# Performance work log

Hardware: AMD Instinct MI355X
Metric: run time of the kernel (lower is better)

Reference implementation:

```python
import jax, jax.numpy as jnp
import numpy as np

N_NODES = 100000
N_EDGES = 1600000
IN_C, HID_C, OUT_C = 128, 128, 40


def setup_inputs() -> dict:
    key = jax.random.key(0)
    ks = jax.random.split(key, 8)
    sd_in = 1.0 / np.sqrt(IN_C)
    sd_hid = 1.0 / np.sqrt(HID_C)
    return {
        "x": jax.random.normal(ks[0], (N_NODES, IN_C), dtype=jnp.float32),
        "edge_index": jax.random.randint(ks[1], (2, N_EDGES), 0, N_NODES, dtype=jnp.int64),
        # layer 1: lin_l (aggregated neighbors, with bias), lin_r (root, no bias)
        "W1l": jax.random.uniform(ks[2], (IN_C, HID_C), jnp.float32, -sd_in, sd_in),
        "W1r": jax.random.uniform(ks[3], (IN_C, HID_C), jnp.float32, -sd_in, sd_in),
        "b1": jnp.zeros((HID_C,), jnp.float32),
        # layer 2
        "W2l": jax.random.uniform(ks[4], (HID_C, OUT_C), jnp.float32, -sd_hid, sd_hid),
        "W2r": jax.random.uniform(ks[5], (HID_C, OUT_C), jnp.float32, -sd_hid, sd_hid),
        "b2": jnp.zeros((OUT_C,), jnp.float32),
    }


def _sage_conv(x, src, dst, Wl, Wr, b, num_nodes):
    # mean aggregation of source-node messages at destination nodes
    msg = x[src]                                          # [E, d] gather
    agg = jax.ops.segment_sum(msg, dst, num_segments=num_nodes)  # [N, d]
    cnt = jax.ops.segment_sum(jnp.ones((src.shape[0],), x.dtype), dst,
                              num_segments=num_nodes)     # [N]
    agg = agg / jnp.maximum(cnt, 1.0)[:, None]
    # lin_l(agg) + lin_r(x)  (bias lives in lin_l, matching PyG SAGEConv)
    return agg @ Wl + x @ Wr + b


def reference(x, edge_index, W1l, W1r, b1, W2l, W2r, b2):
    n = x.shape[0]
    src, dst = edge_index[0], edge_index[1]  # messages flow src -> dst
    h = jax.nn.relu(_sage_conv(x, src, dst, W1l, W1r, b1, n))
    # dropout p=0.0 -> identity
    out = _sage_conv(h, src, dst, W2l, W2r, b2, n)
    return jax.nn.log_softmax(out, axis=-1)
```

## Files before the change

### kernel.cpp

```cpp
#include <hip/hip_runtime.h>
#include <stdint.h>


typedef unsigned int uint32;
typedef unsigned short u16;
typedef __bf16 bf16x8 __attribute__((ext_vector_type(8)));
typedef float  f32x4  __attribute__((ext_vector_type(4)));
typedef unsigned short u16x8 __attribute__((ext_vector_type(8)));

#define CAPB 96
#define MAXE 2592
#define MAXN 104
#define RSST 112

__device__ __forceinline__ float bf2f(u16 u) {
    union { uint32 i; float f; } v; v.i = ((uint32)u) << 16; return v.f;
}
__device__ __forceinline__ u16 f2bf(float f) {
    union { float f; uint32 i; } v; v.f = f;
    uint32 i = v.i;
    uint32 r = (i + 0x7FFFu + ((i >> 16) & 1u)) >> 16;
    return (u16)r;
}

__global__ void k_prep(const float* __restrict__ W1l, const float* __restrict__ W1r,
                       const float* __restrict__ W2l, const float* __restrict__ W2r,
                       u16* __restrict__ Wt1, u16* __restrict__ Wt2,
                       int* __restrict__ gcur1, int cap1,
                       int* __restrict__ gcur2, int cap2) {
    if (blockIdx.x == 0 && threadIdx.x < 8) gcur1[threadIdx.x] = threadIdx.x * cap1;
    if (blockIdx.x < 4) {
        int idx = blockIdx.x * 256 + threadIdx.x;
        gcur2[idx] = idx * cap2;
    }
    if (blockIdx.x < 128) {
        int idx = blockIdx.x * 256 + threadIdx.x;
        int c = idx >> 7, k = idx & 127;
        float v = (c < 128) ? W1l[k * 128 + c] : W1r[k * 128 + (c - 128)];
        Wt1[idx] = f2bf(v);
    } else {
        int idx = (blockIdx.x - 128) * 256 + threadIdx.x;
        int c = idx >> 7, k = idx & 127;
        const float* W = (c < 48) ? W2l : W2r;
        int cc = (c < 48) ? c : c - 48;
        float v = (cc < 40) ? W[k * 40 + cc] : 0.f;
        Wt2[idx] = f2bf(v);
    }
}

__global__ __launch_bounds__(512) void k_fused1(
        const int* __restrict__ src, const int* __restrict__ dst,
        uint32* __restrict__ part, int* __restrict__ gcur,
        int E, int sw, uint32 magic, int cap, int nt1,
        const float* __restrict__ x, const u16* __restrict__ Wt,
        u16* __restrict__ z1, u16* __restrict__ r1, int N) {
    int tid = threadIdx.x;
    if ((int)blockIdx.x < nt1) {
        __shared__ uint32 buf[2048];
        __shared__ int cnt8[8][8];
        __shared__ int base8[8][8];
        __shared__ int bstart[8], bn[8], gbase[8];
        int rep = tid & 7;
        int tile = blockIdx.x;
        if (tid < 64) cnt8[tid >> 3][tid & 7] = 0;
        __syncthreads();
        int e0 = (tile << 11) + tid * 4;
        int bk[4]; uint32 pk[4]; int nv = 0;
        if (e0 + 3 < E) {
            int4 d4 = *(const int4*)(dst + e0);
            int4 s4 = *(const int4*)(src + e0);
            int dd[4] = {d4.x, d4.y, d4.z, d4.w};
            int ss[4] = {s4.x, s4.y, s4.z, s4.w};
            nv = 4;
#pragma unroll
            for (int k = 0; k < 4; ++k) {
                bk[k] = (int)(((unsigned long long)(uint32)dd[k] * magic) >> 32);
                pk[k] = ((uint32)ss[k] << 14) | (uint32)(dd[k] - bk[k] * sw);
            }
        } else {
            for (int e = e0; e < E && e < e0 + 4; ++e) {
                int d = dst[e];
                int b = (int)(((unsigned long long)(uint32)d * magic) >> 32);
                bk[nv] = b;
                pk[nv] = ((uint32)src[e] << 14) | (uint32)(d - b * sw);
                ++nv;
            }
        }
        for (int k = 0; k < nv; ++k) atomicAdd(&cnt8[bk[k]][rep], 1);
        __syncthreads();
        if (tid == 0) {
            int run = 0;
            for (int b = 0; b < 8; ++b) {
                bstart[b] = run; int t0 = run;
                for (int r = 0; r < 8; ++r) { base8[b][r] = run; run += cnt8[b][r]; }
                bn[b] = run - t0;
            }
        }
        __syncthreads();
        if (tid < 64) cnt8[tid >> 3][tid & 7] = base8[tid >> 3][tid & 7];
        __syncthreads();
        for (int k = 0; k < nv; ++k) {
            int pos = atomicAdd(&cnt8[bk[k]][rep], 1);
            buf[pos] = pk[k];
        }
        if (tid < 8 && bn[tid] > 0)
            gbase[tid] = atomicAdd(&gcur[tid], bn[tid]);
        __syncthreads();
#pragma unroll
        for (int b = 0; b < 8; ++b) {
            int n = bn[b];
            if (n == 0) continue;
            int gb = gbase[b], bs = bstart[b];
            int lim = (b + 1) * cap;
            for (int i = tid; i < n; i += 512) {
                int p = gb + i;
                if (p < lim) part[p] = buf[bs + i];
            }
        }
    } else {
        __shared__ u16 xs[128][136];
        int rbase = ((int)blockIdx.x - nt1) * 128;
#pragma unroll
        for (int i = 0; i < 8; ++i) {
            int fi = tid + i * 512;
            int row = fi >> 5, c4 = fi & 31;
            int grow = rbase + row;
            grow = grow < N ? grow : N - 1;
            float4 v = *(const float4*)(x + ((size_t)grow << 7) + c4 * 4);
            ushort4 w4;
            w4.x = f2bf(v.x); w4.y = f2bf(v.y); w4.z = f2bf(v.z); w4.w = f2bf(v.w);
            *(ushort4*)&xs[row][c4 * 4] = w4;
        }

        int lane = tid & 63;
        int w    = tid >> 6;
        int l15 = lane & 15, g = lane >> 4;
        int rloc = (w >> 2) * 64;
        int cbase = (w & 3) * 64;

        bf16x8 Bf[4][4];
#pragma unroll
        for (int c = 0; c < 4; ++c)
#pragma unroll
            for (int ks = 0; ks < 4; ++ks)
                Bf[c][ks] = *(const bf16x8*)(Wt + (((size_t)(cbase + c * 16 + l15)) << 7)
                                                + ks * 32 + g * 8);

        f32x4 acc[4][4];
        f32x4 z4 = {0.f, 0.f, 0.f, 0.f};
#pragma unroll
        for (int r = 0; r < 4; ++r)
#pragma unroll
            for (int c = 0; c < 4; ++c) acc[r][c] = z4;

        __syncthreads();

#pragma unroll
        for (int ks = 0; ks < 4; ++ks) {
            bf16x8 Af[4];
#pragma unroll
            for (int r = 0; r < 4; ++r)
                Af[r] = *(const bf16x8*)&xs[rloc + r * 16 + l15][ks * 32 + g * 8];
#pragma unroll
            for (int r = 0; r < 4; ++r)
#pragma unroll
                for (int c = 0; c < 4; ++c)
                    acc[r][c] = __builtin_amdgcn_mfma_f32_16x16x32_bf16(
                                    Af[r], Bf[c][ks], acc[r][c], 0, 0, 0);
        }

#pragma unroll
        for (int r = 0; r < 4; ++r) {
#pragma unroll
            for (int c = 0; c < 4; ++c) {
                int col = cbase + c * 16 + l15;
                u16* out = (col < 128) ? z1 : r1;
                int cc = col & 127;
#pragma unroll
                for (int j = 0; j < 4; ++j) {
                    int row = rbase + rloc + r * 16 + g * 4 + j;
                    if (row < N) out[((size_t)row << 7) + cc] = f2bf(acc[r][c][j]);
                }
            }
        }
    }
}

__global__ __launch_bounds__(256) void k_part2(const uint32* __restrict__ part1,
        const int* __restrict__ gcur1, uint32* __restrict__ part2,
        int* __restrict__ gcur2, int cap1, int cap2, int sw2, uint32 magic2) {
    __shared__ uint32 buf[128][CAPB];
    __shared__ int lcnt[128], gbase[128];
    int s = blockIdx.x & 7;
    int m = gcur1[s] - s * cap1;
    const uint32* p1 = part1 + (size_t)s * cap1;
    int sbase = s * 128;
    int ntiles = (m + 4095) >> 12;
    for (int tile = blockIdx.x >> 3; tile < ntiles; tile += (gridDim.x >> 3)) {
        for (int i = threadIdx.x; i < 128; i += 256) lcnt[i] = 0;
        __syncthreads();
#pragma unroll
        for (int q = 0; q < 4; ++q) {
            int t0 = (tile << 12) + q * 1024 + threadIdx.x * 4;
            if (t0 + 3 < m) {
                uint4 v4 = *(const uint4*)(p1 + t0);
                uint32 vv[4] = {v4.x, v4.y, v4.z, v4.w};
#pragma unroll
                for (int k = 0; k < 4; ++k) {
                    uint32 dl = vv[k] & 16383u;
                    int sub = (int)(((unsigned long long)dl * magic2) >> 32);
                    uint32 pk = ((vv[k] >> 14) << 7) | (dl - (uint32)(sub * sw2));
                    int slot = atomicAdd(&lcnt[sub], 1);
                    if (slot < CAPB) buf[sub][slot] = pk;
                    else {
                        int p = atomicAdd(&gcur2[sbase + sub], 1);
                        if (p < (sbase + sub + 1) * cap2) part2[p] = pk;
                    }
                }
            } else {
                for (int idx = t0; idx < m && idx < t0 + 4; ++idx) {
                    uint32 v = p1[idx];
                    uint32 dl = v & 16383u;
                    int sub = (int)(((unsigned long long)dl * magic2) >> 32);
                    uint32 pk = ((v >> 14) << 7) | (dl - (uint32)(sub * sw2));
                    int slot = atomicAdd(&lcnt[sub], 1);
                    if (slot < CAPB) buf[sub][slot] = pk;
                    else {
                        int p = atomicAdd(&gcur2[sbase + sub], 1);
                        if (p < (sbase + sub + 1) * cap2) part2[p] = pk;
                    }
                }
            }
        }
        __syncthreads();
        if (threadIdx.x < 128) {
            int n = min(lcnt[threadIdx.x], CAPB);
            lcnt[threadIdx.x] = n;
            if (n > 0) gbase[threadIdx.x] = atomicAdd(&gcur2[sbase + threadIdx.x], n);
        }
        __syncthreads();
        int b = threadIdx.x >> 1, halfsel = threadIdx.x & 1;
        int n = lcnt[b];
        if (n > 0) {
            int gb = gbase[b];
            int lim = (sbase + b + 1) * cap2;
            for (int i = halfsel; i < n; i += 2) {
                int p = gb + i;
                if (p < lim) part2[p] = buf[b][i];
            }
        }
        __syncthreads();
    }
}

__global__ __launch_bounds__(256) void k_gemm2(const u16* __restrict__ hb,
        const u16* __restrict__ Wt2,
        u16* __restrict__ z2p, u16* __restrict__ r2, int N) {
    __shared__ u16 hs[128][136];
    int tid = threadIdx.x;
    int rbase = blockIdx.x * 128;
#pragma unroll
    for (int i = 0; i < 8; ++i) {
        int ci = tid + i * 256;
        int row = ci >> 4, c8 = ci & 15;
        int grow = rbase + row;
        grow = grow < N ? grow : N - 1;
        u16x8 v = *(const u16x8*)(hb + ((size_t)grow << 7) + c8 * 8);
        *(u16x8*)&hs[row][c8 * 8] = v;
    }

    int lane = tid & 63;
    int w    = tid >> 6;
    int l15 = lane & 15, g = lane >> 4;
    int rloc = (w >> 1) * 64;
    int half = w & 1;

    bf16x8 Bf[3][4];
#pragma unroll
    for (int c = 0; c < 3; ++c)
#pragma unroll
        for (int ks = 0; ks < 4; ++ks)
            Bf[c][ks] = *(const bf16x8*)(Wt2 + (((size_t)(half * 48 + c * 16 + l15)) << 7)
                                             + ks * 32 + g * 8);

    f32x4 acc[4][3];
    f32x4 z4 = {0.f, 0.f, 0.f, 0.f};
#pragma unroll
    for (int r = 0; r < 4; ++r)
#pragma unroll
        for (int c = 0; c < 3; ++c) acc[r][c] = z4;

    __syncthreads();

#pragma unroll
    for (int ks = 0; ks < 4; ++ks) {
        bf16x8 Af[4];
#pragma unroll
        for (int r = 0; r < 4; ++r)
            Af[r] = *(const bf16x8*)&hs[rloc + r * 16 + l15][ks * 32 + g * 8];
#pragma unroll
        for (int r = 0; r < 4; ++r)
#pragma unroll
            for (int c = 0; c < 3; ++c)
                acc[r][c] = __builtin_amdgcn_mfma_f32_16x16x32_bf16(
                                Af[r], Bf[c][ks], acc[r][c], 0, 0, 0);
    }

    if (half == 0) {
#pragma unroll
        for (int r = 0; r < 4; ++r)
#pragma unroll
            for (int c = 0; c < 3; ++c) {
                int col = c * 16 + l15;
#pragma unroll
                for (int j = 0; j < 4; ++j) {
                    int row = rbase + rloc + r * 16 + g * 4 + j;
                    if (row < N) z2p[((size_t)row << 6) + col] = f2bf(acc[r][c][j]);
                }
            }
        int row = rbase + rloc + lane;
        if (row < N) {
            u16x8 z8 = {0, 0, 0, 0, 0, 0, 0, 0};
            *(u16x8*)(z2p + ((size_t)row << 6) + 48) = z8;
            *(u16x8*)(z2p + ((size_t)row << 6) + 56) = z8;
        }
    } else {
#pragma unroll
        for (int r = 0; r < 4; ++r)
#pragma unroll
            for (int c = 0; c < 3; ++c) {
                int col = c * 16 + l15;
                if (col < 40) {
#pragma unroll
                    for (int j = 0; j < 4; ++j) {
                        int row = rbase + rloc + r * 16 + g * 4 + j;
                        if (row < N) r2[(size_t)row * 40 + col] = f2bf(acc[r][c][j]);
                    }
                }
            }
    }
}

__global__ __launch_bounds__(512) void k_agg1_f(const u16* __restrict__ z1,
        const u16* __restrict__ r1, const float* __restrict__ b1,
        uint32* __restrict__ part2, const int* __restrict__ gcur2,
        u16* __restrict__ h, int* __restrict__ rsg,
        int N, int sw1, int sw2, int cap2) {
    __shared__ uint32 ebuf[MAXE];
    __shared__ uint32 esrt[MAXE];
    __shared__ int cnt[MAXN], cur[MAXN], rs[MAXN + 32];
    int b = blockIdx.x, s = b >> 7, sub = b & 127;
    int nb = s * sw1 + sub * sw2;
    int slice_end = min((s + 1) * sw1, N);
    int nn = min(sw2, slice_end - nb);
    if (nn <= 0) return;
    int tid = threadIdx.x;
    int m2 = gcur2[b] - b * cap2;
    m2 = min(m2, min(cap2, MAXE));
    uint32* p2 = part2 + (size_t)b * cap2;

    for (int i = tid; i < m2; i += 512) ebuf[i] = p2[i];
    for (int i = tid; i < nn; i += 512) cnt[i] = 0;
    __syncthreads();
    for (int i = tid; i < m2; i += 512) atomicAdd(&cnt[ebuf[i] & 127], 1);
    __syncthreads();
    if (tid < 64) {
        int c0 = (tid < nn) ? cnt[tid] : 0;
        int c1 = (64 + tid < nn) ? cnt[64 + tid] : 0;
        for (int off = 1; off < 64; off <<= 1) {
            int t0 = __shfl_up(c0, off, 64);
            int t1 = __shfl_up(c1, off, 64);
            if (tid >= off) { c0 += t0; c1 += t1; }
        }
        int tot0 = __shfl(c0, 63, 64);
        if (tid == 0) rs[0] = 0;
        rs[tid + 1] = c0;
        rs[64 + tid + 1] = tot0 + c1;
    }
    __syncthreads();
    for (int i = tid; i < nn; i += 512) cur[i] = rs[i];
    __syncthreads();
    for (int i = tid; i < m2; i += 512) {
        uint32 v = ebuf[i];
        int pos = atomicAdd(&cur[v & 127], 1);
        esrt[pos] = v >> 7;
    }
    __syncthreads();

    for (int i = tid; i < m2; i += 512) p2[i] = esrt[i];
    for (int i = tid; i <= nn; i += 512) rsg[b * RSST + i] = rs[i];

    int lane = tid & 63, wv = tid >> 6;
    int g = lane >> 4, c = lane & 15;
    for (int node = wv; node < nn; node += 8) {
        int s0 = rs[node], s1 = rs[node + 1];
        float acc[8];
#pragma unroll
        for (int i = 0; i < 8; ++i) acc[i] = 0.f;
        int j = s0 + g;
        for (; j + 12 < s1; j += 16) {
            int sA = esrt[j], sB = esrt[j + 4];
            int sC = esrt[j + 8], sD = esrt[j + 12];
            u16x8 a = *(const u16x8*)(z1 + ((size_t)sA << 7) + c * 8);
            u16x8 bb = *(const u16x8*)(z1 + ((size_t)sB << 7) + c * 8);
            u16x8 d = *(const u16x8*)(z1 + ((size_t)sC << 7) + c * 8);
            u16x8 e = *(const u16x8*)(z1 + ((size_t)sD << 7) + c * 8);
#pragma unroll
            for (int i = 0; i < 8; ++i)
                acc[i] += (bf2f(a[i]) + bf2f(bb[i])) + (bf2f(d[i]) + bf2f(e[i]));
        }
        for (; j + 4 < s1; j += 8) {
            int sA = esrt[j], sB = esrt[j + 4];
            u16x8 a = *(const u16x8*)(z1 + ((size_t)sA << 7) + c * 8);
            u16x8 bb = *(const u16x8*)(z1 + ((size_t)sB << 7) + c * 8);
#pragma unroll
            for (int i = 0; i < 8; ++i) acc[i] += bf2f(a[i]) + bf2f(bb[i]);
        }
        if (j < s1) {
            int sA = esrt[j];
            u16x8 a = *(const u16x8*)(z1 + ((size_t)sA << 7) + c * 8);
#pragma unroll
            for (int i = 0; i < 8; ++i) acc[i] += bf2f(a[i]);
        }
#pragma unroll
        for (int i = 0; i < 8; ++i) {
            acc[i] += __shfl_xor(acc[i], 16, 64);
            acc[i] += __shfl_xor(acc[i], 32, 64);
        }
        if (g == 0) {
            float inv = 1.0f / fmaxf((float)(s1 - s0), 1.0f);
            size_t go = ((size_t)(nb + node) << 7) + c * 8;
            u16x8 rv = *(const u16x8*)(r1 + go);
            float4 b0 = *(const float4*)(b1 + c * 8);
            float4 b4 = *(const float4*)(b1 + c * 8 + 4);
            float bbv[8] = {b0.x, b0.y, b0.z, b0.w, b4.x, b4.y, b4.z, b4.w};
            u16x8 o;
#pragma unroll
            for (int i = 0; i < 8; ++i)
                o[i] = f2bf(fmaxf(acc[i] * inv + bf2f(rv[i]) + bbv[i], 0.f));
            *(u16x8*)(h + go) = o;
        }
    }
}

__global__ __launch_bounds__(512) void k_agg2_f(const u16* __restrict__ z2p,
        const u16* __restrict__ r2, const float* __restrict__ b2,
        const uint32* __restrict__ part2, const int* __restrict__ gcur2,
        const int* __restrict__ rsg, float* __restrict__ out,
        int N, int sw1, int sw2, int cap2) {
    __shared__ uint32 esrt[MAXE];
    __shared__ int rs[MAXN + 1];
    int b = blockIdx.x, s = b >> 7, sub = b & 127;
    int nb = s * sw1 + sub * sw2;
    int slice_end = min((s + 1) * sw1, N);
    int nn = min(sw2, slice_end - nb);
    if (nn <= 0) return;
    int tid = threadIdx.x;
    int m2 = gcur2[b] - b * cap2;
    m2 = min(m2, min(cap2, MAXE));
    const uint32* p2 = part2 + (size_t)b * cap2;

    for (int i = tid; i < m2; i += 512) esrt[i] = p2[i];
    for (int i = tid; i <= nn; i += 512) rs[i] = rsg[b * RSST + i];
    __syncthreads();

    int lane = tid & 63, wv = tid >> 6;
    int le = lane >> 3, c = lane & 7;
    bool act = c < 5;
    for (int node = wv; node < nn; node += 8) {
        int s0 = rs[node], s1 = rs[node + 1];
        float acc[8];
#pragma unroll
        for (int i = 0; i < 8; ++i) acc[i] = 0.f;
        int j = s0 + le;
        for (; j + 8 < s1; j += 16) {
            int sA = esrt[j], sB = esrt[j + 8];
            u16x8 a = *(const u16x8*)(z2p + ((size_t)sA << 6) + c * 8);
            u16x8 bb = *(const u16x8*)(z2p + ((size_t)sB << 6) + c * 8);
#pragma unroll
            for (int i = 0; i < 8; ++i) acc[i] += bf2f(a[i]) + bf2f(bb[i]);
        }
        if (j < s1) {
            int sA = esrt[j];
            u16x8 a = *(const u16x8*)(z2p + ((size_t)sA << 6) + c * 8);
#pragma unroll
            for (int i = 0; i < 8; ++i) acc[i] += bf2f(a[i]);
        }
#pragma unroll
        for (int i = 0; i < 8; ++i) {
            acc[i] += __shfl_xor(acc[i], 8, 64);
            acc[i] += __shfl_xor(acc[i], 16, 64);
            acc[i] += __shfl_xor(acc[i], 32, 64);
        }
        if (le == 0) {
            float inv = 1.0f / fmaxf((float)(s1 - s0), 1.0f);
            float v[8];
            if (act) {
                u16x8 rv = *(const u16x8*)(r2 + (size_t)(nb + node) * 40 + c * 8);
                float4 b0 = *(const float4*)(b2 + c * 8);
                float4 b4 = *(const float4*)(b2 + c * 8 + 4);
                float bbv[8] = {b0.x, b0.y, b0.z, b0.w, b4.x, b4.y, b4.z, b4.w};
#pragma unroll
                for (int i = 0; i < 8; ++i) v[i] = acc[i] * inv + bf2f(rv[i]) + bbv[i];
            } else {
#pragma unroll
                for (int i = 0; i < 8; ++i) v[i] = -1e30f;
            }
            float m = v[0];
#pragma unroll
            for (int i = 1; i < 8; ++i) m = fmaxf(m, v[i]);
            m = fmaxf(m, __shfl_xor(m, 1, 64));
            m = fmaxf(m, __shfl_xor(m, 2, 64));
            m = fmaxf(m, __shfl_xor(m, 4, 64));
            float sum = 0.f;
            if (act) {
#pragma unroll
                for (int i = 0; i < 8; ++i) sum += __expf(v[i] - m);
            }
            sum += __shfl_xor(sum, 1, 64);
            sum += __shfl_xor(sum, 2, 64);
            sum += __shfl_xor(sum, 4, 64);
            float lse = __logf(sum);
            if (act) {
                float4 o0, o4;
                o0.x = v[0] - m - lse; o0.y = v[1] - m - lse;
                o0.z = v[2] - m - lse; o0.w = v[3] - m - lse;
                o4.x = v[4] - m - lse; o4.y = v[5] - m - lse;
                o4.z = v[6] - m - lse; o4.w = v[7] - m - lse;
                *(float4*)(out + (size_t)(nb + node) * 40 + c * 8) = o0;
                *(float4*)(out + (size_t)(nb + node) * 40 + c * 8 + 4) = o4;
            }
        }
    }
}

extern "C" void kernel_launch(void* const* d_in, const int* in_sizes, int n_in,
                              void* d_out, int out_size, void* d_ws, size_t ws_size,
                              hipStream_t stream) {
    const float* x   = (const float*)d_in[0];
    const int*   ei  = (const int*)d_in[1];
    const float* W1l = (const float*)d_in[2];
    const float* W1r = (const float*)d_in[3];
    const float* b1  = (const float*)d_in[4];
    const float* W2l = (const float*)d_in[5];
    const float* W2r = (const float*)d_in[6];
    const float* b2  = (const float*)d_in[7];
    float* out = (float*)d_out;

    int N = in_sizes[0] / 128;
    int E = in_sizes[1] / 2;
    const int* esrc = ei;
    const int* edst = ei + E;

    int sw1 = (N + 7) / 8;
    int sw2 = (sw1 + 127) / 128;
    uint32 magic1 = (uint32)((((unsigned long long)1 << 32) + sw1 - 1) / sw1);
    uint32 magic2 = (uint32)((((unsigned long long)1 << 32) + sw2 - 1) / sw2);
    int cap1 = (((E >> 3) + 8192) + 3) & ~3;
    int cap2 = (((E >> 10) + 1024) + 3) & ~3;

    char* p = (char*)d_ws;
    size_t off = 0;
    auto alloc = [&](size_t bytes) {
        void* q = p + off;
        off = (off + bytes + 255) & ~(size_t)255;
        return q;
    };
    int* gcur1 = (int*)alloc(64);
    int* gcur2 = (int*)alloc(1024 * 4);
    int* rsg   = (int*)alloc((size_t)1024 * RSST * 4);
    u16* Wt1 = (u16*)alloc(256 * 128 * 2);
    u16* Wt2 = (u16*)alloc(96 * 128 * 2);
    uint32* part1 = (uint32*)alloc((size_t)8 * cap1 * 4);
    uint32* part2 = (uint32*)alloc((size_t)1024 * cap2 * 4);
    u16* z1 = (u16*)alloc((size_t)N * 128 * 2);
    u16* r1 = (u16*)alloc((size_t)N * 128 * 2);
    u16* hb = r1;
    u16* z2p = z1;
    u16* r2  = z1 + (size_t)N * 64;

    int nt1 = (E + 2047) >> 11;
    int ng1 = (N + 127) / 128;

    k_prep<<<176, 256, 0, stream>>>(W1l, W1r, W2l, W2r, Wt1, Wt2,
                                    gcur1, cap1, gcur2, cap2);
    k_fused1<<<nt1 + ng1, 512, 0, stream>>>(esrc, edst, part1, gcur1,
                                            E, sw1, magic1, cap1, nt1,
                                            x, Wt1, z1, r1, N);
    k_part2<<<392, 256, 0, stream>>>(part1, gcur1, part2, gcur2, cap1, cap2,
                                     sw2, magic2);
    k_agg1_f<<<1024, 512, 0, stream>>>(z1, r1, b1, part2, gcur2, hb, rsg,
                                       N, sw1, sw2, cap2);
    k_gemm2<<<(N + 127) / 128, 256, 0, stream>>>(hb, Wt2, z2p, r2, N);
    k_agg2_f<<<1024, 512, 0, stream>>>(z2p, r2, b2, part2, gcur2, rsg, out,
                                       N, sw1, sw2, cap2);
}
```

Baseline: 183.4 us.

## Fuse layer-2 GEMM into layer-1 aggregation kernel via shared-memory hidden tile

The layer-1 aggregation kernel now keeps its ReLU'd hidden rows in shared memory instead of writing them to global. It then runs the layer-2 MFMA projection (Wl and Wr halves) directly on that tile and writes z2p and r2. This drops the separate k_gemm2 launch and the global round trip of the hidden matrix. In exchange it uses more shared memory per block (the edge buffer is aliased onto the hidden tile), loads B fragments from global inside the loop, and allocates separate z2p/r2 buffers.

Measured after the change: 197.3 us (median of 2 runs). 1.08x slower.

```diff
diff --git a/kernel.cpp b/kernel.cpp
--- a/kernel.cpp
+++ b/kernel.cpp
@@ -253,102 +253,15 @@
     }
 }
 
-__global__ __launch_bounds__(256) void k_gemm2(const u16* __restrict__ hb,
-        const u16* __restrict__ Wt2,
-        u16* __restrict__ z2p, u16* __restrict__ r2, int N) {
-    __shared__ u16 hs[128][136];
-    int tid = threadIdx.x;
-    int rbase = blockIdx.x * 128;
-#pragma unroll
-    for (int i = 0; i < 8; ++i) {
-        int ci = tid + i * 256;
-        int row = ci >> 4, c8 = ci & 15;
-        int grow = rbase + row;
-        grow = grow < N ? grow : N - 1;
-        u16x8 v = *(const u16x8*)(hb + ((size_t)grow << 7) + c8 * 8);
-        *(u16x8*)&hs[row][c8 * 8] = v;
-    }
-
-    int lane = tid & 63;
-    int w    = tid >> 6;
-    int l15 = lane & 15, g = lane >> 4;
-    int rloc = (w >> 1) * 64;
-    int half = w & 1;
-
-    bf16x8 Bf[3][4];
-#pragma unroll
-    for (int c = 0; c < 3; ++c)
-#pragma unroll
-        for (int ks = 0; ks < 4; ++ks)
-            Bf[c][ks] = *(const bf16x8*)(Wt2 + (((size_t)(half * 48 + c * 16 + l15)) << 7)
-                                             + ks * 32 + g * 8);
-
-    f32x4 acc[4][3];
-    f32x4 z4 = {0.f, 0.f, 0.f, 0.f};
-#pragma unroll
-    for (int r = 0; r < 4; ++r)
-#pragma unroll
-        for (int c = 0; c < 3; ++c) acc[r][c] = z4;
-
-    __syncthreads();
-
-#pragma unroll
-    for (int ks = 0; ks < 4; ++ks) {
-        bf16x8 Af[4];
-#pragma unroll
-        for (int r = 0; r < 4; ++r)
-            Af[r] = *(const bf16x8*)&hs[rloc + r * 16 + l15][ks * 32 + g * 8];
-#pragma unroll
-        for (int r = 0; r < 4; ++r)
-#pragma unroll
-            for (int c = 0; c < 3; ++c)
-                acc[r][c] = __builtin_amdgcn_mfma_f32_16x16x32_bf16(
-                                Af[r], Bf[c][ks], acc[r][c], 0, 0, 0);
-    }
-
-    if (half == 0) {
-#pragma unroll
-        for (int r = 0; r < 4; ++r)
-#pragma unroll
-            for (int c = 0; c < 3; ++c) {
-                int col = c * 16 + l15;
-#pragma unroll
-                for (int j = 0; j < 4; ++j) {
-                    int row = rbase + rloc + r * 16 + g * 4 + j;
-                    if (row < N) z2p[((size_t)row << 6) + col] = f2bf(acc[r][c][j]);
-                }
-            }
-        int row = rbase + rloc + lane;
-        if (row < N) {
-            u16x8 z8 = {0, 0, 0, 0, 0, 0, 0, 0};
-            *(u16x8*)(z2p + ((size_t)row << 6) + 48) = z8;
-            *(u16x8*)(z2p + ((size_t)row << 6) + 56) = z8;
-        }
-    } else {
-#pragma unroll
-        for (int r = 0; r < 4; ++r)
-#pragma unroll
-            for (int c = 0; c < 3; ++c) {
-                int col = c * 16 + l15;
-                if (col < 40) {
-#pragma unroll
-                    for (int j = 0; j < 4; ++j) {
-                        int row = rbase + rloc + r * 16 + g * 4 + j;
-                        if (row < N) r2[(size_t)row * 40 + col] = f2bf(acc[r][c][j]);
-                    }
-                }
-            }
-    }
-}
-
-__global__ __launch_bounds__(512) void k_agg1_f(const u16* __restrict__ z1,
+__global__ __launch_bounds__(512) void k_agg1g2(const u16* __restrict__ z1,
         const u16* __restrict__ r1, const float* __restrict__ b1,
         uint32* __restrict__ part2, const int* __restrict__ gcur2,
-        u16* __restrict__ h, int* __restrict__ rsg,
-        int N, int sw1, int sw2, int cap2) {
-    __shared__ uint32 ebuf[MAXE];
+        const u16* __restrict__ Wt2, u16* __restrict__ z2p, u16* __restrict__ r2,
+        int* __restrict__ rsg, int N, int sw1, int sw2, int cap2) {
+    __shared__ u16 hs[112][136];
     __shared__ uint32 esrt[MAXE];
     __shared__ int cnt[MAXN], cur[MAXN], rs[MAXN + 32];
+    uint32* ebuf = (uint32*)&hs[0][0];
     int b = blockIdx.x, s = b >> 7, sub = b & 127;
     int nb = s * sw1 + sub * sw2;
     int slice_end = min((s + 1) * sw1, N);
@@ -438,8 +351,54 @@
 #pragma unroll
             for (int i = 0; i < 8; ++i)
                 o[i] = f2bf(fmaxf(acc[i] * inv + bf2f(rv[i]) + bbv[i], 0.f));
-            *(u16x8*)(h + go) = o;
-        }
+            *(u16x8*)&hs[node][c * 8] = o;
+        }
+    }
+    {
+        int r0 = nn + (tid >> 4), cc = tid & 15;
+        u16x8 z8 = {0, 0, 0, 0, 0, 0, 0, 0};
+        for (int r = r0; r < 112; r += 32) *(u16x8*)&hs[r][cc * 8] = z8;
+    }
+    __syncthreads();
+
+    int l15 = lane & 15;
+    if (wv < 7 && wv * 16 < nn) {
+        f32x4 acc6[6];
+        f32x4 z4 = {0.f, 0.f, 0.f, 0.f};
+#pragma unroll
+        for (int cf = 0; cf < 6; ++cf) acc6[cf] = z4;
+#pragma unroll
+        for (int ks = 0; ks < 4; ++ks) {
+            bf16x8 Af = *(const bf16x8*)&hs[wv * 16 + l15][ks * 32 + g * 8];
+#pragma unroll
+            for (int cf = 0; cf < 6; ++cf) {
+                bf16x8 Bf = *(const bf16x8*)(Wt2 + (((size_t)(cf * 16 + l15)) << 7)
+                                                 + ks * 32 + g * 8);
+                acc6[cf] = __builtin_amdgcn_mfma_f32_16x16x32_bf16(
+                               Af, Bf, acc6[cf], 0, 0, 0);
+            }
+        }
+#pragma unroll
+        for (int cf = 0; cf < 6; ++cf) {
+#pragma unroll
+            for (int j = 0; j < 4; ++j) {
+                int lr = wv * 16 + g * 4 + j;
+                if (lr >= nn) continue;
+                int grow = nb + lr;
+                if (cf < 3) {
+                    int col = cf * 16 + l15;
+                    z2p[((size_t)grow << 6) + col] = f2bf(acc6[cf][j]);
+                } else {
+                    int col = (cf - 3) * 16 + l15;
+                    if (col < 40)
+                        r2[(size_t)grow * 40 + col] = f2bf(acc6[cf][j]);
+                }
+            }
+        }
+    }
+    for (int r = tid >> 1; r < nn; r += 256) {
+        u16x8 z8 = {0, 0, 0, 0, 0, 0, 0, 0};
+        *(u16x8*)(z2p + (((size_t)(nb + r)) << 6) + 48 + (tid & 1) * 8) = z8;
     }
 }
 
@@ -575,9 +534,8 @@
     uint32* part2 = (uint32*)alloc((size_t)1024 * cap2 * 4);
     u16* z1 = (u16*)alloc((size_t)N * 128 * 2);
     u16* r1 = (u16*)alloc((size_t)N * 128 * 2);
-    u16* hb = r1;
-    u16* z2p = z1;
-    u16* r2  = z1 + (size_t)N * 64;
+    u16* z2p = (u16*)alloc((size_t)N * 64 * 2);
+    u16* r2  = (u16*)alloc((size_t)N * 40 * 2);
 
     int nt1 = (E + 2047) >> 11;
     int ng1 = (N + 127) / 128;
@@ -589,9 +547,8 @@
                                             x, Wt1, z1, r1, N);
     k_part2<<<392, 256, 0, stream>>>(part1, gcur1, part2, gcur2, cap1, cap2,
                                      sw2, magic2);
-    k_agg1_f<<<1024, 512, 0, stream>>>(z1, r1, b1, part2, gcur2, hb, rsg,
-                                       N, sw1, sw2, cap2);
-    k_gemm2<<<(N + 127) / 128, 256, 0, stream>>>(hb, Wt2, z2p, r2, N);
+    k_agg1g2<<<1024, 512, 0, stream>>>(z1, r1, b1, part2, gcur2,
+                                       Wt2, z2p, r2, rsg, N, sw1, sw2, cap2);
     k_agg2_f<<<1024, 512, 0, stream>>>(z2p, r2, b2, part2, gcur2, rsg, out,
                                        N, sw1, sw2, cap2);
 }
```
